# Kernel tuning notes

Hardware: AMD Instinct MI355X
Metric: run time of the kernel (lower is better)

The kernel has to match this reference:

```python
import jax, jax.numpy as jnp
import numpy as np

B, N, C = 8, 2048, 512

def setup_inputs() -> dict:
    key = jax.random.key(0)
    k1, k2, k3 = jax.random.split(key, 3)
    x = jax.random.normal(k1, (B, N, C), dtype=jnp.float32)
    # xavier_uniform with gain=1.414 ~ uniform(-b, b), b = gain*sqrt(6/(fan_in+fan_out))
    bw = 1.414 * np.sqrt(6.0 / (C + C))
    w = jax.random.uniform(k2, (C, C), dtype=jnp.float32, minval=-bw, maxval=bw)
    ba = 1.414 * np.sqrt(6.0 / (2 * C + 1))
    a = jax.random.uniform(k3, (2 * C, 1), dtype=jnp.float32, minval=-ba, maxval=ba)
    return {"x": x, "w": w, "a": a}

def reference(x, w, a):
    # x: [B,N,C], w: [C,C], a: [2C,1]
    C_ = w.shape[0]
    h = jnp.matmul(x, w)                      # [B,N,C]
    a1 = a[:C_, 0]                            # [C]
    a2 = a[C_:, 0]                            # [C]
    # The torch repeat/cat/view builds e_ij = LeakyReLU(a1.h_i + a2.h_j);
    # compute the same math via broadcasting (no [B,N,N,2C] tensor).
    s1 = jnp.einsum('bnc,c->bn', h, a1)       # [B,N]
    s2 = jnp.einsum('bnc,c->bn', h, a2)       # [B,N]
    e = jax.nn.leaky_relu(s1[:, :, None] + s2[:, None, :], negative_slope=0.2)  # [B,N,N]
    attention = jax.nn.softmax(e, axis=2)     # softmax over source nodes j
    # dropout is identity in eval mode (training=False)
    h_prime = jnp.matmul(attention, x)        # [B,N,C]
    return h_prime
```

## Files before the change

kernel.cpp:

```cpp
#include <hip/hip_runtime.h>
#include <math.h>

#define B_ 8
#define N_ 2048
#define C_ 512
#define G_ 32
#define L_ 64

static const size_t OFF_V1   = 0;
static const size_t OFF_V2   = OFF_V1 + 512;
static const size_t OFF_S1   = OFF_V2 + 512;
static const size_t OFF_S2   = OFF_S1 + 16384;
static const size_t OFF_Z    = OFF_S2 + 16384;
static const size_t OFF_IDX  = OFF_Z + 16384;
static const size_t OFF_P    = OFF_IDX + 16384;
static const size_t OFF_Q    = OFF_P + 16384;
static const size_t OFF_PPRE = OFF_Q + 16384;
static const size_t OFF_QPRE = OFF_PPRE + 16400;
static const size_t OFF_CHP  = OFF_QPRE + 16400;
static const size_t OFF_CHQ  = OFF_CHP + 131072;
static const size_t OFF_TOTQ = OFF_CHQ + 131072;
static const size_t OFF_BIGE = OFF_TOTQ + 4096;

__global__ __launch_bounds__(64) void k_wa(const float* __restrict__ w,
                                           const float* __restrict__ a,
                                           float* __restrict__ v1, float* __restrict__ v2) {
    int k = blockIdx.x, lane = threadIdx.x;
    float acc1 = 0.f, acc2 = 0.f;
    for (int c = lane; c < C_; c += 64) {
        float wv = w[k * C_ + c];
        acc1 += wv * a[c];
        acc2 += wv * a[C_ + c];
    }
    for (int o = 32; o > 0; o >>= 1) { acc1 += __shfl_down(acc1, o); acc2 += __shfl_down(acc2, o); }
    if (lane == 0) { v1[k] = acc1; v2[k] = acc2; }
}

__global__ __launch_bounds__(256) void k_s(const float* __restrict__ x,
                                           const float* __restrict__ v1,
                                           const float* __restrict__ v2,
                                           float* __restrict__ s1, float* __restrict__ s2) {
    __shared__ __align__(16) float sv1[C_];
    __shared__ __align__(16) float sv2[C_];
    int tid = threadIdx.x;
    for (int c = tid; c < C_; c += 256) { sv1[c] = v1[c]; sv2[c] = v2[c]; }
    __syncthreads();
    int wave = tid >> 6, lane = tid & 63;
    int r = blockIdx.x * 4 + wave;
    const float4* xr  = reinterpret_cast<const float4*>(x + (size_t)r * C_);
    const float4* w1p = reinterpret_cast<const float4*>(sv1);
    const float4* w2p = reinterpret_cast<const float4*>(sv2);
    float a1 = 0.f, a2 = 0.f;
    for (int half = 0; half < 2; ++half) {
        int c4 = lane + half * 64;
        float4 xv = xr[c4], w1 = w1p[c4], w2 = w2p[c4];
        a1 += xv.x*w1.x + xv.y*w1.y + xv.z*w1.z + xv.w*w1.w;
        a2 += xv.x*w2.x + xv.y*w2.y + xv.z*w2.z + xv.w*w2.w;
    }
    for (int o = 32; o > 0; o >>= 1) { a1 += __shfl_down(a1, o); a2 += __shfl_down(a2, o); }
    if (lane == 0) { s1[r] = a1; s2[r] = a2; }
}

__global__ __launch_bounds__(256) void k_rank(const float* __restrict__ s2,
                                              float* __restrict__ z, int* __restrict__ idxArr,
                                              float* __restrict__ pArr, float* __restrict__ qArr) {
    __shared__ float sval[N_];
    __shared__ float sred[256];
    __shared__ int   srnk[256];
    int blk = blockIdx.x;
    int b = blk >> 5, grp = blk & 31;
    int tid = threadIdx.x;
    int le = tid & 63, qtr = tid >> 6;
    for (int i = tid; i < N_; i += 256) sval[i] = s2[(size_t)b * N_ + i];
    __syncthreads();
    int e = grp * 64 + le;
    float val = sval[e];
    int base = qtr * 512;
    int rank = 0;
    float mx = -3.4e38f;
    #pragma unroll 8
    for (int i = 0; i < 512; ++i) {
        int t = base + i;
        float v = sval[t];
        mx = fmaxf(mx, v);
        rank += (v < val) || (v == val && t < e);
    }
    srnk[tid] = rank;
    sred[tid] = mx;
    __syncthreads();
    for (int o = 128; o > 0; o >>= 1) {
        if (tid < o) sred[tid] = fmaxf(sred[tid], sred[tid + o]);
        __syncthreads();
    }
    float m2 = sred[0];
    if (qtr == 0) {
        int rk = srnk[le] + srnk[le + 64] + srnk[le + 128] + srnk[le + 192];
        float d = val - m2;
        size_t pos = (size_t)b * N_ + rk;
        z[pos]      = val;
        idxArr[pos] = e;
        pArr[pos]   = __expf(d);
        qArr[pos]   = __expf(0.2f * d);
    }
}

__global__ __launch_bounds__(1024) void k_scan(const float* __restrict__ pArr,
                                               const float* __restrict__ qArr,
                                               float* __restrict__ Ppre, float* __restrict__ Qpre) {
    __shared__ float wsP[16], wsQ[16], woP[16], woQ[16];
    int b = blockIdx.x, tid = threadIdx.x, lane = tid & 63, wid = tid >> 6;
    size_t ib = (size_t)b * N_;
    float p0 = pArr[ib + 2 * tid], p1 = pArr[ib + 2 * tid + 1];
    float q0 = qArr[ib + 2 * tid], q1 = qArr[ib + 2 * tid + 1];
    float pv = p0 + p1, qv = q0 + q1;
    float pi = pv, qi = qv;
    for (int o = 1; o < 64; o <<= 1) {
        float tp = __shfl_up(pi, o), tq = __shfl_up(qi, o);
        if (lane >= o) { pi += tp; qi += tq; }
    }
    if (lane == 63) { wsP[wid] = pi; wsQ[wid] = qi; }
    __syncthreads();
    if (wid == 0 && lane < 16) {
        float sp = wsP[lane], sq = wsQ[lane];
        float ip = sp, iq = sq;
        for (int o = 1; o < 16; o <<= 1) {
            float tp = __shfl_up(ip, o), tq = __shfl_up(iq, o);
            if (lane >= o) { ip += tp; iq += tq; }
        }
        woP[lane] = ip - sp; woQ[lane] = iq - sq;
    }
    __syncthreads();
    float inclP = pi + woP[wid], inclQ = qi + woQ[wid];
    float exclP = inclP - pv, exclQ = inclQ - qv;
    size_t base = (size_t)b * 2049;
    Ppre[base + 2 * tid]     = exclP;
    Ppre[base + 2 * tid + 1] = exclP + p0;
    Qpre[base + 2 * tid]     = exclQ;
    Qpre[base + 2 * tid + 1] = exclQ + q0;
    if (tid == 1023) { Ppre[base + N_] = inclP; Qpre[base + N_] = inclQ; }
}

__global__ __launch_bounds__(512) void k_chunk(const float* __restrict__ x,
                                               const int* __restrict__ idxArr,
                                               const float* __restrict__ pArr,
                                               const float* __restrict__ qArr,
                                               float* __restrict__ chP, float* __restrict__ chQ) {
    int bg = blockIdx.x, b = bg >> 5, g = bg & 31;
    int c = threadIdx.x;
    __shared__ int   srow[L_];
    __shared__ float spv[L_], sqv[L_];
    if (c < L_) {
        int j = g * L_ + c;
        srow[c] = idxArr[b * N_ + j];
        spv[c]  = pArr[b * N_ + j];
        sqv[c]  = qArr[b * N_ + j];
    }
    __syncthreads();
    const float* xb = x + (size_t)b * N_ * C_;
    float accP = 0.f, accQ = 0.f;
    for (int t = 0; t < L_; ++t) {
        float xv = xb[(size_t)srow[t] * C_ + c];
        accP += spv[t] * xv;
        accQ += sqv[t] * xv;
    }
    chP[(size_t)bg * C_ + c] = accP;
    chQ[(size_t)bg * C_ + c] = accQ;
}

__global__ __launch_bounds__(512) void k_choff(float* __restrict__ chP, float* __restrict__ chQ,
                                               float* __restrict__ totQ) {
    int b = blockIdx.x, c = threadIdx.x;
    float vP[G_], vQ[G_];
    #pragma unroll
    for (int g = 0; g < G_; ++g) {
        size_t id = ((size_t)(b * G_ + g)) * C_ + c;
        vP[g] = chP[id];
        vQ[g] = chQ[id];
    }
    float runP = 0.f, runQ = 0.f;
    #pragma unroll
    for (int g = G_ - 1; g >= 0; --g) {
        size_t id = ((size_t)(b * G_ + g)) * C_ + c;
        float tP = vP[g], tQ = vQ[g];
        chP[id] = runP; chQ[id] = runQ;
        runP += tP; runQ += tQ;
    }
    totQ[b * C_ + c] = runQ;
}

__global__ __launch_bounds__(512) void k_cumsum(const float* __restrict__ x,
                                                const int* __restrict__ idxArr,
                                                const float* __restrict__ pArr,
                                                const float* __restrict__ qArr,
                                                const float* __restrict__ chP,
                                                const float* __restrict__ chQ,
                                                const float* __restrict__ totQ,
                                                float2* __restrict__ bigE) {
    int bg = blockIdx.x, b = bg >> 5, g = bg & 31;
    int c = threadIdx.x;
    __shared__ int   srow[L_];
    __shared__ float spv[L_], sqv[L_];
    if (c < L_) {
        int j = g * L_ + c;
        srow[c] = idxArr[b * N_ + j];
        spv[c]  = pArr[b * N_ + j];
        sqv[c]  = qArr[b * N_ + j];
    }
    __syncthreads();
    const float* xb = x + (size_t)b * N_ * C_;
    float runP = chP[(size_t)bg * C_ + c];
    float runQ = chQ[(size_t)bg * C_ + c];
    float tq   = totQ[b * C_ + c];
    float2* bigEb = bigE + (size_t)b * (N_ + 1) * C_;
    if (g == G_ - 1) bigEb[(size_t)N_ * C_ + c] = make_float2(0.f, tq);
    for (int t = L_ - 1; t >= 0; --t) {
        int j = g * L_ + t;
        float xv = xb[(size_t)srow[t] * C_ + c];
        runP += spv[t] * xv;
        runQ += sqv[t] * xv;
        bigEb[(size_t)j * C_ + c] = make_float2(runP, tq - runQ);
    }
}

__global__ __launch_bounds__(256) void k_out(const float* __restrict__ s1,
                                             const float* __restrict__ z,
                                             const float* __restrict__ Ppre,
                                             const float* __restrict__ Qpre,
                                             const float2* __restrict__ bigE,
                                             float* __restrict__ out) {
    int tid = threadIdx.x, wave = tid >> 6, lane = tid & 63;
    int r = blockIdx.x * 4 + wave;
    int b = r >> 11;
    float s1v = s1[r];
    const float* zb = z + (size_t)b * N_;
    float m2  = zb[N_ - 1];
    float thr = -s1v;
    int lo = 0, hi = N_;
    while (lo < hi) {
        int mid = (lo + hi) >> 1;
        if (zb[mid] >= thr) hi = mid; else lo = mid + 1;
    }
    int k = lo;
    float beta = s1v + m2;
    float wP, wQ;
    if (beta >= 0.f) { wP = 1.f;                 wQ = __expf(-0.8f * beta); }
    else             { wP = __expf(0.8f * beta); wQ = 1.f; }
    float Sp = Ppre[b * 2049 + N_] - Ppre[b * 2049 + k];
    float Sq = Qpre[b * 2049 + k];
    float inv = 1.0f / (wP * Sp + wQ * Sq);
    float fP = wP * inv, fQ = wQ * inv;
    const float4* row4 = reinterpret_cast<const float4*>(bigE + ((size_t)b * (N_ + 1) + k) * C_);
    float2* orow = reinterpret_cast<float2*>(out + (size_t)r * C_);
    #pragma unroll
    for (int half = 0; half < 4; ++half) {
        int c4 = lane + half * 64;
        float4 E = row4[c4];
        orow[c4] = make_float2(fP * E.x + fQ * E.y, fP * E.z + fQ * E.w);
    }
}

extern "C" void kernel_launch(void* const* d_in, const int* in_sizes, int n_in,
                              void* d_out, int out_size, void* d_ws, size_t ws_size,
                              hipStream_t stream) {
    const float* x = (const float*)d_in[0];
    const float* w = (const float*)d_in[1];
    const float* a = (const float*)d_in[2];
    float* out = (float*)d_out;
    float* ws  = (float*)d_ws;

    float*  v1   = ws + OFF_V1;
    float*  v2   = ws + OFF_V2;
    float*  s1   = ws + OFF_S1;
    float*  s2   = ws + OFF_S2;
    float*  zArr = ws + OFF_Z;
    int*    idxA = (int*)(ws + OFF_IDX);
    float*  pArr = ws + OFF_P;
    float*  qArr = ws + OFF_Q;
    float*  Ppre = ws + OFF_PPRE;
    float*  Qpre = ws + OFF_QPRE;
    float*  chP  = ws + OFF_CHP;
    float*  chQ  = ws + OFF_CHQ;
    float*  totQ = ws + OFF_TOTQ;
    float2* bigE = (float2*)(ws + OFF_BIGE);

    k_wa    <<<dim3(C_),      dim3(64),   0, stream>>>(w, a, v1, v2);
    k_s     <<<dim3(4096),    dim3(256),  0, stream>>>(x, v1, v2, s1, s2);
    k_rank  <<<dim3(B_ * 32), dim3(256),  0, stream>>>(s2, zArr, idxA, pArr, qArr);
    k_scan  <<<dim3(B_),      dim3(1024), 0, stream>>>(pArr, qArr, Ppre, Qpre);
    k_chunk <<<dim3(B_ * G_), dim3(512),  0, stream>>>(x, idxA, pArr, qArr, chP, chQ);
    k_choff <<<dim3(B_),      dim3(512),  0, stream>>>(chP, chQ, totQ);
    k_cumsum<<<dim3(B_ * G_), dim3(512),  0, stream>>>(x, idxA, pArr, qArr, chP, chQ, totQ, bigE);
    k_out   <<<dim3(4096),    dim3(256),  0, stream>>>(s1, zArr, Ppre, Qpre, bigE, out);
}
```

Before: 148.8 us.

## Fuse cumsum and output via bucketed rows, drop bigE intermediate

Removes the large float2 bigE buffer ([B,N+1,C]) that was written by the cumsum kernel and read back by the output kernel. A new prep kernel merges the prefix scans, chunk offsets and per-row binary search. It also buckets the query rows by split index using a counting sort in shared memory. The fused kernel then writes each output row directly when the running cumulative sum reaches that row's bucket. This saves roughly 2x 67MB of global traffic and two launches, at the cost of scattered row writes and a single 8-block prep kernel with low parallelism.

Result: slower. 152.3 us (+2.4%).

```diff
diff --git a/kernel.cpp b/kernel.cpp
--- a/kernel.cpp
+++ b/kernel.cpp
@@ -15,12 +15,13 @@
 static const size_t OFF_IDX  = OFF_Z + 16384;
 static const size_t OFF_P    = OFF_IDX + 16384;
 static const size_t OFF_Q    = OFF_P + 16384;
-static const size_t OFF_PPRE = OFF_Q + 16384;
-static const size_t OFF_QPRE = OFF_PPRE + 16400;
-static const size_t OFF_CHP  = OFF_QPRE + 16400;
+static const size_t OFF_CHP  = OFF_Q + 16384;
 static const size_t OFF_CHQ  = OFF_CHP + 131072;
 static const size_t OFF_TOTQ = OFF_CHQ + 131072;
-static const size_t OFF_BIGE = OFF_TOTQ + 4096;
+static const size_t OFF_FP   = OFF_TOTQ + 4096;
+static const size_t OFF_FQ   = OFF_FP + 16384;
+static const size_t OFF_ROWS = OFF_FQ + 16384;
+static const size_t OFF_POS  = OFF_ROWS + 16384;
 
 __global__ __launch_bounds__(64) void k_wa(const float* __restrict__ w,
                                            const float* __restrict__ a,
@@ -102,42 +103,6 @@
         pArr[pos]   = __expf(d);
         qArr[pos]   = __expf(0.2f * d);
     }
-}
-
-__global__ __launch_bounds__(1024) void k_scan(const float* __restrict__ pArr,
-                                               const float* __restrict__ qArr,
-                                               float* __restrict__ Ppre, float* __restrict__ Qpre) {
-    __shared__ float wsP[16], wsQ[16], woP[16], woQ[16];
-    int b = blockIdx.x, tid = threadIdx.x, lane = tid & 63, wid = tid >> 6;
-    size_t ib = (size_t)b * N_;
-    float p0 = pArr[ib + 2 * tid], p1 = pArr[ib + 2 * tid + 1];
-    float q0 = qArr[ib + 2 * tid], q1 = qArr[ib + 2 * tid + 1];
-    float pv = p0 + p1, qv = q0 + q1;
-    float pi = pv, qi = qv;
-    for (int o = 1; o < 64; o <<= 1) {
-        float tp = __shfl_up(pi, o), tq = __shfl_up(qi, o);
-        if (lane >= o) { pi += tp; qi += tq; }
-    }
-    if (lane == 63) { wsP[wid] = pi; wsQ[wid] = qi; }
-    __syncthreads();
-    if (wid == 0 && lane < 16) {
-        float sp = wsP[lane], sq = wsQ[lane];
-        float ip = sp, iq = sq;
-        for (int o = 1; o < 16; o <<= 1) {
-            float tp = __shfl_up(ip, o), tq = __shfl_up(iq, o);
-            if (lane >= o) { ip += tp; iq += tq; }
-        }
-        woP[lane] = ip - sp; woQ[lane] = iq - sq;
-    }
-    __syncthreads();
-    float inclP = pi + woP[wid], inclQ = qi + woQ[wid];
-    float exclP = inclP - pv, exclQ = inclQ - qv;
-    size_t base = (size_t)b * 2049;
-    Ppre[base + 2 * tid]     = exclP;
-    Ppre[base + 2 * tid + 1] = exclP + p0;
-    Qpre[base + 2 * tid]     = exclQ;
-    Qpre[base + 2 * tid + 1] = exclQ + q0;
-    if (tid == 1023) { Ppre[base + N_] = inclP; Qpre[base + N_] = inclQ; }
 }
 
 __global__ __launch_bounds__(512) void k_chunk(const float* __restrict__ x,
@@ -167,95 +132,175 @@
     chQ[(size_t)bg * C_ + c] = accQ;
 }
 
-__global__ __launch_bounds__(512) void k_choff(float* __restrict__ chP, float* __restrict__ chQ,
-                                               float* __restrict__ totQ) {
-    int b = blockIdx.x, c = threadIdx.x;
-    float vP[G_], vQ[G_];
+__global__ __launch_bounds__(1024) void k_prep(const float* __restrict__ s1,
+                                               const float* __restrict__ z,
+                                               const float* __restrict__ pArr,
+                                               const float* __restrict__ qArr,
+                                               float* __restrict__ chP,
+                                               float* __restrict__ chQ,
+                                               float* __restrict__ totQ,
+                                               float* __restrict__ fPArr,
+                                               float* __restrict__ fQArr,
+                                               int* __restrict__ rowsSorted,
+                                               int* __restrict__ posStart) {
+    __shared__ float Ppre[2049], Qpre[2049];
+    __shared__ float zv[N_];
+    __shared__ int   cnt[2049];
+    __shared__ int   ps[2050];
+    __shared__ float wsP[16], wsQ[16], woP[16], woQ[16];
+    __shared__ int   wsC[16], woC[16];
+    int b = blockIdx.x, tid = threadIdx.x, lane = tid & 63, wid = tid >> 6;
+    size_t ib = (size_t)b * N_;
+
+    for (int i = tid; i < 2049; i += 1024) cnt[i] = 0;
+    zv[2*tid]   = z[ib + 2*tid];
+    zv[2*tid+1] = z[ib + 2*tid+1];
+
+    float p0 = pArr[ib + 2*tid], p1 = pArr[ib + 2*tid+1];
+    float q0 = qArr[ib + 2*tid], q1 = qArr[ib + 2*tid+1];
+    float pv = p0 + p1, qv = q0 + q1;
+    float pi = pv, qi = qv;
+    for (int o = 1; o < 64; o <<= 1) {
+        float tp = __shfl_up(pi, o), tq2 = __shfl_up(qi, o);
+        if (lane >= o) { pi += tp; qi += tq2; }
+    }
+    if (lane == 63) { wsP[wid] = pi; wsQ[wid] = qi; }
+    __syncthreads();
+    if (wid == 0 && lane < 16) {
+        float sp = wsP[lane], sq = wsQ[lane];
+        float ip = sp, iq = sq;
+        for (int o = 1; o < 16; o <<= 1) {
+            float tp = __shfl_up(ip, o), tq2 = __shfl_up(iq, o);
+            if (lane >= o) { ip += tp; iq += tq2; }
+        }
+        woP[lane] = ip - sp; woQ[lane] = iq - sq;
+    }
+    {
+        int c = tid & 511, sel = tid >> 9;
+        float* arr = sel ? chQ : chP;
+        float v[G_];
+        #pragma unroll
+        for (int g = 0; g < G_; ++g)
+            v[g] = arr[((size_t)(b * G_ + g)) * C_ + c];
+        float run = 0.f;
+        #pragma unroll
+        for (int g = G_ - 1; g >= 0; --g) {
+            float t = v[g];
+            arr[((size_t)(b * G_ + g)) * C_ + c] = run;
+            run += t;
+        }
+        if (sel) totQ[b * C_ + c] = run;
+    }
+    __syncthreads();
+    float inclP = pi + woP[wid], inclQ = qi + woQ[wid];
+    float exclP = inclP - pv,    exclQ = inclQ - qv;
+    Ppre[2*tid]   = exclP;  Ppre[2*tid+1] = exclP + p0;
+    Qpre[2*tid]   = exclQ;  Qpre[2*tid+1] = exclQ + q0;
+    if (tid == 1023) { Ppre[2048] = inclP; Qpre[2048] = inclQ; }
+    __syncthreads();
+
+    float m2   = zv[N_ - 1];
+    float Ptot = Ppre[2048];
+    int kk[2], sl[2];
     #pragma unroll
-    for (int g = 0; g < G_; ++g) {
-        size_t id = ((size_t)(b * G_ + g)) * C_ + c;
-        vP[g] = chP[id];
-        vQ[g] = chQ[id];
-    }
-    float runP = 0.f, runQ = 0.f;
+    for (int h = 0; h < 2; ++h) {
+        int rl = tid + h * 1024;
+        float s1v = s1[ib + rl];
+        float thr = -s1v;
+        int lo = 0, hi = N_;
+        while (lo < hi) { int mid = (lo + hi) >> 1; if (zv[mid] >= thr) hi = mid; else lo = mid + 1; }
+        float beta = s1v + m2;
+        float wPc, wQc;
+        if (beta >= 0.f) { wPc = 1.f;                  wQc = __expf(-0.8f * beta); }
+        else             { wPc = __expf(0.8f * beta);  wQc = 1.f; }
+        float Sp = Ptot - Ppre[lo];
+        float Sq = Qpre[lo];
+        float inv = 1.f / (wPc * Sp + wQc * Sq);
+        fPArr[ib + rl] = wPc * inv;
+        fQArr[ib + rl] = wQc * inv;
+        kk[h] = lo;
+        sl[h] = atomicAdd(&cnt[lo], 1);
+    }
+    __syncthreads();
+
+    int c0 = cnt[2*tid], c1 = cnt[2*tid+1];
+    int cv = c0 + c1, ci = cv;
+    for (int o = 1; o < 64; o <<= 1) {
+        int t = __shfl_up(ci, o);
+        if (lane >= o) ci += t;
+    }
+    if (lane == 63) wsC[wid] = ci;
+    __syncthreads();
+    if (wid == 0 && lane < 16) {
+        int sc = wsC[lane], ic = sc;
+        for (int o = 1; o < 16; o <<= 1) { int t = __shfl_up(ic, o); if (lane >= o) ic += t; }
+        woC[lane] = ic - sc;
+    }
+    __syncthreads();
+    int inclC = ci + woC[wid];
+    int exclC = inclC - cv;
+    ps[2*tid] = exclC; ps[2*tid+1] = exclC + c0;
+    if (tid == 1023) { ps[2048] = inclC; ps[2049] = inclC + cnt[2048]; }
+    __syncthreads();
+    posStart[b * 2050 + tid]        = ps[tid];
+    posStart[b * 2050 + 1024 + tid] = ps[1024 + tid];
+    if (tid < 2) posStart[b * 2050 + 2048 + tid] = ps[2048 + tid];
     #pragma unroll
-    for (int g = G_ - 1; g >= 0; --g) {
-        size_t id = ((size_t)(b * G_ + g)) * C_ + c;
-        float tP = vP[g], tQ = vQ[g];
-        chP[id] = runP; chQ[id] = runQ;
-        runP += tP; runQ += tQ;
-    }
-    totQ[b * C_ + c] = runQ;
-}
-
-__global__ __launch_bounds__(512) void k_cumsum(const float* __restrict__ x,
-                                                const int* __restrict__ idxArr,
-                                                const float* __restrict__ pArr,
-                                                const float* __restrict__ qArr,
-                                                const float* __restrict__ chP,
-                                                const float* __restrict__ chQ,
-                                                const float* __restrict__ totQ,
-                                                float2* __restrict__ bigE) {
+    for (int h = 0; h < 2; ++h) {
+        int rl = tid + h * 1024;
+        rowsSorted[ib + ps[kk[h]] + sl[h]] = rl;
+    }
+}
+
+__global__ __launch_bounds__(512) void k_fused(const float* __restrict__ x,
+                                               const int* __restrict__ idxArr,
+                                               const float* __restrict__ pArr,
+                                               const float* __restrict__ qArr,
+                                               const float* __restrict__ chP,
+                                               const float* __restrict__ chQ,
+                                               const float* __restrict__ totQ,
+                                               const float* __restrict__ fPArr,
+                                               const float* __restrict__ fQArr,
+                                               const int* __restrict__ rowsSorted,
+                                               const int* __restrict__ posStart,
+                                               float* __restrict__ out) {
     int bg = blockIdx.x, b = bg >> 5, g = bg & 31;
     int c = threadIdx.x;
     __shared__ int   srow[L_];
     __shared__ float spv[L_], sqv[L_];
+    __shared__ int   sps[66];
     if (c < L_) {
         int j = g * L_ + c;
         srow[c] = idxArr[b * N_ + j];
         spv[c]  = pArr[b * N_ + j];
         sqv[c]  = qArr[b * N_ + j];
     }
-    __syncthreads();
-    const float* xb = x + (size_t)b * N_ * C_;
+    if (c < 66) sps[c] = posStart[b * 2050 + g * L_ + c];
+    __syncthreads();
+    const float* xb  = x + (size_t)b * N_ * C_;
+    const float* fPb = fPArr + (size_t)b * N_;
+    const float* fQb = fQArr + (size_t)b * N_;
+    const int*   rs  = rowsSorted + (size_t)b * N_;
+    float*       ob  = out + (size_t)b * N_ * C_;
     float runP = chP[(size_t)bg * C_ + c];
     float runQ = chQ[(size_t)bg * C_ + c];
     float tq   = totQ[b * C_ + c];
-    float2* bigEb = bigE + (size_t)b * (N_ + 1) * C_;
-    if (g == G_ - 1) bigEb[(size_t)N_ * C_ + c] = make_float2(0.f, tq);
+    if (g == G_ - 1) {
+        for (int u = sps[64]; u < sps[65]; ++u) {
+            int r = rs[u];
+            ob[(size_t)r * C_ + c] = fPb[r] * runP + fQb[r] * (tq - runQ);
+        }
+    }
+    float xv_next = xb[(size_t)srow[L_ - 1] * C_ + c];
     for (int t = L_ - 1; t >= 0; --t) {
-        int j = g * L_ + t;
-        float xv = xb[(size_t)srow[t] * C_ + c];
-        runP += spv[t] * xv;
-        runQ += sqv[t] * xv;
-        bigEb[(size_t)j * C_ + c] = make_float2(runP, tq - runQ);
-    }
-}
-
-__global__ __launch_bounds__(256) void k_out(const float* __restrict__ s1,
-                                             const float* __restrict__ z,
-                                             const float* __restrict__ Ppre,
-                                             const float* __restrict__ Qpre,
-                                             const float2* __restrict__ bigE,
-                                             float* __restrict__ out) {
-    int tid = threadIdx.x, wave = tid >> 6, lane = tid & 63;
-    int r = blockIdx.x * 4 + wave;
-    int b = r >> 11;
-    float s1v = s1[r];
-    const float* zb = z + (size_t)b * N_;
-    float m2  = zb[N_ - 1];
-    float thr = -s1v;
-    int lo = 0, hi = N_;
-    while (lo < hi) {
-        int mid = (lo + hi) >> 1;
-        if (zb[mid] >= thr) hi = mid; else lo = mid + 1;
-    }
-    int k = lo;
-    float beta = s1v + m2;
-    float wP, wQ;
-    if (beta >= 0.f) { wP = 1.f;                 wQ = __expf(-0.8f * beta); }
-    else             { wP = __expf(0.8f * beta); wQ = 1.f; }
-    float Sp = Ppre[b * 2049 + N_] - Ppre[b * 2049 + k];
-    float Sq = Qpre[b * 2049 + k];
-    float inv = 1.0f / (wP * Sp + wQ * Sq);
-    float fP = wP * inv, fQ = wQ * inv;
-    const float4* row4 = reinterpret_cast<const float4*>(bigE + ((size_t)b * (N_ + 1) + k) * C_);
-    float2* orow = reinterpret_cast<float2*>(out + (size_t)r * C_);
-    #pragma unroll
-    for (int half = 0; half < 4; ++half) {
-        int c4 = lane + half * 64;
-        float4 E = row4[c4];
-        orow[c4] = make_float2(fP * E.x + fQ * E.y, fP * E.z + fQ * E.w);
+        float xv = xv_next;
+        if (t > 0) xv_next = xb[(size_t)srow[t - 1] * C_ + c];
+        runP = fmaf(spv[t], xv, runP);
+        runQ = fmaf(sqv[t], xv, runQ);
+        for (int u = sps[t]; u < sps[t + 1]; ++u) {
+            int r = rs[u];
+            ob[(size_t)r * C_ + c] = fPb[r] * runP + fQb[r] * (tq - runQ);
+        }
     }
 }
 
@@ -268,27 +313,28 @@
     float* out = (float*)d_out;
     float* ws  = (float*)d_ws;
 
-    float*  v1   = ws + OFF_V1;
-    float*  v2   = ws + OFF_V2;
-    float*  s1   = ws + OFF_S1;
-    float*  s2   = ws + OFF_S2;
-    float*  zArr = ws + OFF_Z;
-    int*    idxA = (int*)(ws + OFF_IDX);
-    float*  pArr = ws + OFF_P;
-    float*  qArr = ws + OFF_Q;
-    float*  Ppre = ws + OFF_PPRE;
-    float*  Qpre = ws + OFF_QPRE;
-    float*  chP  = ws + OFF_CHP;
-    float*  chQ  = ws + OFF_CHQ;
-    float*  totQ = ws + OFF_TOTQ;
-    float2* bigE = (float2*)(ws + OFF_BIGE);
-
-    k_wa    <<<dim3(C_),      dim3(64),   0, stream>>>(w, a, v1, v2);
-    k_s     <<<dim3(4096),    dim3(256),  0, stream>>>(x, v1, v2, s1, s2);
-    k_rank  <<<dim3(B_ * 32), dim3(256),  0, stream>>>(s2, zArr, idxA, pArr, qArr);
-    k_scan  <<<dim3(B_),      dim3(1024), 0, stream>>>(pArr, qArr, Ppre, Qpre);
-    k_chunk <<<dim3(B_ * G_), dim3(512),  0, stream>>>(x, idxA, pArr, qArr, chP, chQ);
-    k_choff <<<dim3(B_),      dim3(512),  0, stream>>>(chP, chQ, totQ);
-    k_cumsum<<<dim3(B_ * G_), dim3(512),  0, stream>>>(x, idxA, pArr, qArr, chP, chQ, totQ, bigE);
-    k_out   <<<dim3(4096),    dim3(256),  0, stream>>>(s1, zArr, Ppre, Qpre, bigE, out);
-}
+    float* v1   = ws + OFF_V1;
+    float* v2   = ws + OFF_V2;
+    float* s1   = ws + OFF_S1;
+    float* s2   = ws + OFF_S2;
+    float* zArr = ws + OFF_Z;
+    int*   idxA = (int*)(ws + OFF_IDX);
+    float* pArr = ws + OFF_P;
+    float* qArr = ws + OFF_Q;
+    float* chP  = ws + OFF_CHP;
+    float* chQ  = ws + OFF_CHQ;
+    float* totQ = ws + OFF_TOTQ;
+    float* fPA  = ws + OFF_FP;
+    float* fQA  = ws + OFF_FQ;
+    int*   rows = (int*)(ws + OFF_ROWS);
+    int*   pos  = (int*)(ws + OFF_POS);
+
+    k_wa   <<<dim3(C_),      dim3(64),   0, stream>>>(w, a, v1, v2);
+    k_s    <<<dim3(4096),    dim3(256),  0, stream>>>(x, v1, v2, s1, s2);
+    k_rank <<<dim3(B_ * 32), dim3(256),  0, stream>>>(s2, zArr, idxA, pArr, qArr);
+    k_chunk<<<dim3(B_ * G_), dim3(512),  0, stream>>>(x, idxA, pArr, qArr, chP, chQ);
+    k_prep <<<dim3(B_),      dim3(1024), 0, stream>>>(s1, zArr, pArr, qArr, chP, chQ, totQ,
+                                                      fPA, fQA, rows, pos);
+    k_fused<<<dim3(B_ * G_), dim3(512),  0, stream>>>(x, idxA, pArr, qArr, chP, chQ, totQ,
+                                                      fPA, fQA, rows, pos, out);
+}
```
